# Kernel tuning notes

Hardware: AMD Instinct MI355X
Metric: run time of the kernel (lower is better)

Reference implementation:

```python
import jax, jax.numpy as jnp
import numpy as np

N_NODES = 50000
N_EDGES = 800000
NODE_DIM = 64
EDGE_DIM = 16
HIDDEN = 128
EPS = 1e-5


def _linear_init(key, fan_in, fan_out):
    k1, k2 = jax.random.split(key)
    bound = 1.0 / np.sqrt(fan_in)
    W = jax.random.uniform(k1, (fan_in, fan_out), minval=-bound, maxval=bound, dtype=jnp.float32)
    b = jax.random.uniform(k2, (fan_out,), minval=-bound, maxval=bound, dtype=jnp.float32)
    return W, b


def batchnorm(h, gamma, beta):
    # BatchNorm1d in training mode: batch mean/var (biased), eps=1e-5
    mu = jnp.mean(h, axis=0, keepdims=True)
    var = jnp.mean((h - mu) ** 2, axis=0, keepdims=True)
    return (h - mu) * jax.lax.rsqrt(var + EPS) * gamma + beta


def setup_inputs() -> dict:
    key = jax.random.key(0)
    ks = jax.random.split(key, 8)
    x = jax.random.normal(ks[0], (N_NODES, NODE_DIM), dtype=jnp.float32)
    edge_index = jax.random.randint(ks[1], (2, N_EDGES), 0, N_NODES, dtype=jnp.int64)
    edge_attr = jax.random.normal(ks[2], (N_EDGES, EDGE_DIM), dtype=jnp.float32)
    We1, be1 = _linear_init(ks[3], 2 * NODE_DIM + EDGE_DIM, HIDDEN)
    We2, be2 = _linear_init(ks[4], HIDDEN, HIDDEN)
    Wm, bm = _linear_init(ks[5], HIDDEN, HIDDEN)
    Wn1, bn1 = _linear_init(ks[6], NODE_DIM + HIDDEN, HIDDEN)
    Wn2, bn2 = _linear_init(ks[7], HIDDEN, HIDDEN)
    ones = jnp.ones((HIDDEN,), jnp.float32)
    zeros = jnp.zeros((HIDDEN,), jnp.float32)
    return dict(x=x, edge_index=edge_index, edge_attr=edge_attr,
                We1=We1, be1=be1, ge=ones, bbe=zeros, We2=We2, be2=be2,
                Wm=Wm, bm=bm,
                Wn1=Wn1, bn1=bn1, gn=ones, bbn=zeros, Wn2=Wn2, bn2=bn2)


def reference(x, edge_index, edge_attr, We1, be1, ge, bbe, We2, be2, Wm, bm, Wn1, bn1, gn, bbn, Wn2, bn2):
    row, col = edge_index[0], edge_index[1]
    # gather + concat -> edge network (Linear, BN, ReLU, Linear)
    edge_input = jnp.concatenate([x[row], x[col], edge_attr], axis=-1)  # [E, 2n+e]
    h = jax.nn.relu(batchnorm(edge_input @ We1 + be1, ge, bbe))
    edge_features = h @ We2 + be2
    # message MLP (Linear, ReLU)
    messages = jax.nn.relu(edge_features @ Wm + bm)  # [E, H]
    # scatter-add into source nodes
    agg = jax.ops.segment_sum(messages, row, num_segments=N_NODES)  # [N, H]
    # node network (Linear, BN, ReLU, Linear)
    node_input = jnp.concatenate([x, agg], axis=-1)
    hn = jax.nn.relu(batchnorm(node_input @ Wn1 + bn1, gn, bbn))
    return hn @ Wn2 + bn2
```

## Files before the change

kernel.cpp:

```cpp
#include <hip/hip_runtime.h>
#include <stdint.h>

#define NNODES 50000
#define NEDGES 800000
#define H 128
#define BN_EPS 1e-5f

typedef short short8 __attribute__((ext_vector_type(8)));
typedef short short4v __attribute__((ext_vector_type(4)));
typedef float f32x4 __attribute__((ext_vector_type(4)));

__device__ __forceinline__ float bf2f(unsigned short u) {
    unsigned int v = ((unsigned int)u) << 16;
    return __uint_as_float(v);
}
__device__ __forceinline__ unsigned short f2bf(float f) {
    unsigned int x = __float_as_uint(f);
    return (unsigned short)((x + 0x7FFFu + ((x >> 16) & 1u)) >> 16);
}
__device__ __forceinline__ short8 s8z() { short8 z = {0,0,0,0,0,0,0,0}; return z; }

template<int KB>
__device__ __forceinline__ void gemm_tile(const short* __restrict__ sA, const int SK,
                                          const unsigned short* __restrict__ WT, const int RK,
                                          const int n0, f32x4 acc[4][4], const int lane) {
    const int mr = lane & 15, quad = lane >> 4;
    const short* W = (const short*)WT;
    #pragma unroll
    for (int kb = 0; kb < KB; ++kb) {
        short8 a[4];
        #pragma unroll
        for (int mt = 0; mt < 4; ++mt)
            a[mt] = *(const short8*)&sA[(mt*16 + mr)*SK + kb*32 + quad*8];
        #pragma unroll
        for (int nt = 0; nt < 4; ++nt) {
            short8 b = *(const short8*)&W[(size_t)(n0 + nt*16 + mr)*RK + kb*32 + quad*8];
            #pragma unroll
            for (int mt = 0; mt < 4; ++mt)
                acc[mt][nt] = __builtin_amdgcn_mfma_f32_16x16x32_bf16(a[mt], b, acc[mt][nt], 0, 0, 0);
        }
    }
}

__global__ void k_fold(const float* __restrict__ We2, const float* __restrict__ be2,
                       const float* __restrict__ Wm, const float* __restrict__ bm,
                       float* __restrict__ W2m, float* __restrict__ b2m) {
    int j = threadIdx.x;
    int i = blockIdx.x;
    if (i < H) {
        float acc = 0.f;
        for (int k = 0; k < H; ++k) acc = fmaf(We2[i*H + k], Wm[k*H + j], acc);
        W2m[i*H + j] = acc;
    } else {
        float acc = bm[j];
        for (int k = 0; k < H; ++k) acc = fmaf(be2[k], Wm[k*H + j], acc);
        b2m[j] = acc;
    }
}

__global__ void k_prep2(const float* __restrict__ We1, const float* __restrict__ Wn1,
                        const float* __restrict__ Wn2,
                        unsigned short* __restrict__ WabT, unsigned short* __restrict__ Wn1T,
                        unsigned short* __restrict__ Wn2T, unsigned short* __restrict__ WcT,
                        int* __restrict__ cnt, float* __restrict__ S1f) {
    int i = blockIdx.x*256 + threadIdx.x;
    if (i < 16384) {
        int n = i >> 6, k = i & 63;
        WabT[n*64 + k] = f2bf(We1[(n < 128 ? k : 64 + k)*H + (n & 127)]);
    } else if (i < 40960) {
        int j = i - 16384; int n = j / 192, k = j - n*192;
        Wn1T[n*192 + k] = f2bf(Wn1[k*H + n]);
    } else if (i < 57344) {
        int j = i - 40960; int n = j >> 7, k = j & 127;
        Wn2T[n*H + k] = f2bf(Wn2[k*H + n]);
    } else if (i < 61440) {
        int j = i - 57344; int n = j >> 5, k = j & 31;
        WcT[n*32 + k] = (k < 16) ? f2bf(We1[(128 + k)*H + n]) : (unsigned short)0;
    } else if (i < 111440) {
        cnt[i - 61440] = 0;
    } else if (i < 112464) {
        S1f[i - 111440] = 0.f;
    }
}

__global__ void k_count(const int* __restrict__ ei, int* __restrict__ cnt) {
    int e = blockIdx.x*256 + threadIdx.x;
    if (e < NEDGES) atomicAdd(&cnt[ei[e]], 1);
}

__global__ void k_scanA(const int* __restrict__ cnt, int* __restrict__ bsum) {
    __shared__ int ws[4];
    const int tid = threadIdx.x;
    int i = blockIdx.x*256 + tid;
    int v = (i < NNODES) ? cnt[i] : 0;
    #pragma unroll
    for (int off = 32; off > 0; off >>= 1) v += __shfl_down(v, off);
    if ((tid & 63) == 0) ws[tid >> 6] = v;
    __syncthreads();
    if (tid == 0) bsum[blockIdx.x] = ws[0] + ws[1] + ws[2] + ws[3];
}

__global__ void k_scanB(const int* __restrict__ bsum, int* __restrict__ bpre,
                        int* __restrict__ offsets) {
    __shared__ int ws[4];
    const int tid = threadIdx.x;
    const int lane = tid & 63, wid = tid >> 6;
    int v = (tid < 196) ? bsum[tid] : 0;
    int xv = v;
    #pragma unroll
    for (int off = 1; off < 64; off <<= 1) {
        int y = __shfl_up(xv, off);
        if (lane >= off) xv += y;
    }
    if (lane == 63) ws[wid] = xv;
    __syncthreads();
    int base = 0;
    for (int w = 0; w < 4; ++w) if (w < wid) base += ws[w];
    int incl = base + xv;
    if (tid < 196) bpre[tid] = incl - v;
    if (tid == 255) offsets[NNODES] = incl;
}

__global__ void k_scanC(const int* __restrict__ cnt, const int* __restrict__ bpre,
                        int* __restrict__ offsets, int* __restrict__ cursor) {
    __shared__ int ws[4];
    const int tid = threadIdx.x;
    const int lane = tid & 63, wid = tid >> 6;
    int i = blockIdx.x*256 + tid;
    int v = (i < NNODES) ? cnt[i] : 0;
    int xv = v;
    #pragma unroll
    for (int off = 1; off < 64; off <<= 1) {
        int y = __shfl_up(xv, off);
        if (lane >= off) xv += y;
    }
    if (lane == 63) ws[wid] = xv;
    __syncthreads();
    int base = bpre[blockIdx.x];
    for (int w = 0; w < 4; ++w) if (w < wid) base += ws[w];
    int excl = base + xv - v;
    if (i < NNODES) { offsets[i] = excl; cursor[i] = excl; }
}

__global__ void k_scatter(const int* __restrict__ ei, int* __restrict__ cursor,
                          int* __restrict__ elist) {
    int e = blockIdx.x*256 + threadIdx.x;
    if (e < NEDGES) {
        int p = atomicAdd(&cursor[ei[e]], 1);
        elist[p] = e;
    }
}

__launch_bounds__(256)
__global__ void k_T(const float* __restrict__ x, const unsigned short* __restrict__ WabT,
                    unsigned short* __restrict__ T) {
    __shared__ short sA[128*72];
    const int tid = threadIdx.x;
    const int n0b = blockIdx.x*128;
    {
        const int rowl = tid >> 1, half = (tid & 1)*32;
        const int node = n0b + rowl;
        const bool ok = node < NNODES;
        #pragma unroll
        for (int c = 0; c < 4; ++c) {
            int k0 = half + c*8;
            short8 o = s8z();
            if (ok) {
                float4 a = *(const float4*)&x[node*64 + k0];
                float4 b = *(const float4*)&x[node*64 + k0 + 4];
                o[0]=(short)f2bf(a.x); o[1]=(short)f2bf(a.y); o[2]=(short)f2bf(a.z); o[3]=(short)f2bf(a.w);
                o[4]=(short)f2bf(b.x); o[5]=(short)f2bf(b.y); o[6]=(short)f2bf(b.z); o[7]=(short)f2bf(b.w);
            }
            *(short8*)&sA[rowl*72 + k0] = o;
        }
    }
    __syncthreads();
    const int wave = tid >> 6, lane = tid & 63;
    const int m0 = (wave & 1)*64;
    const int n0 = blockIdx.y*128 + (wave >> 1)*64;
    f32x4 acc[4][4];
    f32x4 z = {0.f, 0.f, 0.f, 0.f};
    #pragma unroll
    for (int mt = 0; mt < 4; ++mt)
        #pragma unroll
        for (int nt = 0; nt < 4; ++nt) acc[mt][nt] = z;
    gemm_tile<2>(sA + m0*72, 72, WabT, 64, n0, acc, lane);
    const int mr = lane & 15, quad = lane >> 4;
    #pragma unroll
    for (int nt = 0; nt < 4; ++nt) {
        int j = n0 + nt*16 + mr;
        #pragma unroll
        for (int mt = 0; mt < 4; ++mt) {
            int nb = n0b + m0 + mt*16 + quad*4;
            #pragma unroll
            for (int r = 0; r < 4; ++r) {
                int node = nb + r;
                if (node < NNODES) T[(size_t)node*256 + j] = f2bf(acc[mt][nt][r]);
            }
        }
    }
}

__launch_bounds__(256)
__global__ void k_gather3(const unsigned short* __restrict__ T, const int* __restrict__ ei,
                          const int* __restrict__ elist, const float* __restrict__ ea,
                          const unsigned short* __restrict__ WcT, const float* __restrict__ be1,
                          unsigned short* __restrict__ hb,
                          float* __restrict__ gS, float* __restrict__ gSS) {
    __shared__ short sT[128*136];
    __shared__ float sS[H], sSS[H];
    __shared__ int sE[128];
    const int tid = threadIdx.x;
    const int p0 = blockIdx.x*128;
    if (tid < 128) { sS[tid] = 0.f; sSS[tid] = 0.f; sE[tid] = elist[p0 + tid]; }
    __syncthreads();
    const int lp = tid >> 1, half = tid & 1;
    {
        const int e = sE[lp];
        const int row = ei[e], col = ei[NEDGES + e];
        #pragma unroll
        for (int c = 0; c < 8; ++c) {
            int jj = half*64 + c*8;
            short8 t1 = *(const short8*)&T[(size_t)row*256 + jj];
            short8 t2 = *(const short8*)&T[(size_t)col*256 + 128 + jj];
            short8 o;
            #pragma unroll
            for (int i = 0; i < 8; ++i)
                o[i] = (short)f2bf(bf2f((unsigned short)t1[i]) + bf2f((unsigned short)t2[i]));
            *(short8*)&sT[lp*136 + jj] = o;
        }
    }
    const int wave = tid >> 6, lane = tid & 63;
    const int mr = lane & 15, quad = lane >> 4;
    const int mbase = wave*32;
    short8 a0 = s8z(), a1 = s8z();
    if (quad < 2) {
        const float4* ea4 = (const float4*)ea;
        int e0i = sE[mbase + mr];
        int e1i = sE[mbase + 16 + mr];
        float4 u = ea4[(size_t)e0i*4 + quad*2];
        float4 v = ea4[(size_t)e0i*4 + quad*2 + 1];
        a0[0]=(short)f2bf(u.x); a0[1]=(short)f2bf(u.y); a0[2]=(short)f2bf(u.z); a0[3]=(short)f2bf(u.w);
        a0[4]=(short)f2bf(v.x); a0[5]=(short)f2bf(v.y); a0[6]=(short)f2bf(v.z); a0[7]=(short)f2bf(v.w);
        u = ea4[(size_t)e1i*4 + quad*2];
        v = ea4[(size_t)e1i*4 + quad*2 + 1];
        a1[0]=(short)f2bf(u.x); a1[1]=(short)f2bf(u.y); a1[2]=(short)f2bf(u.z); a1[3]=(short)f2bf(u.w);
        a1[4]=(short)f2bf(v.x); a1[5]=(short)f2bf(v.y); a1[6]=(short)f2bf(v.z); a1[7]=(short)f2bf(v.w);
    }
    f32x4 acc[2][8];
    f32x4 z = {0.f, 0.f, 0.f, 0.f};
    #pragma unroll
    for (int mt = 0; mt < 2; ++mt)
        #pragma unroll
        for (int nt = 0; nt < 8; ++nt) acc[mt][nt] = z;
    #pragma unroll
    for (int nt = 0; nt < 8; ++nt) {
        short8 b = *(const short8*)&WcT[(nt*16 + mr)*32 + quad*8];
        acc[0][nt] = __builtin_amdgcn_mfma_f32_16x16x32_bf16(a0, b, acc[0][nt], 0, 0, 0);
        acc[1][nt] = __builtin_amdgcn_mfma_f32_16x16x32_bf16(a1, b, acc[1][nt], 0, 0, 0);
    }
    __syncthreads();
    #pragma unroll
    for (int nt = 0; nt < 8; ++nt) {
        int j = nt*16 + mr;
        float bia = be1[j];
        float s = 0.f, ssum = 0.f;
        #pragma unroll
        for (int mt = 0; mt < 2; ++mt) {
            #pragma unroll
            for (int r = 0; r < 4; ++r) {
                int m = mbase + mt*16 + quad*4 + r;
                float v = acc[mt][nt][r] + bf2f((unsigned short)sT[m*136 + j]) + bia;
                sT[m*136 + j] = (short)f2bf(v);
                s += v; ssum += v*v;
            }
        }
        atomicAdd(&sS[j], s);
        atomicAdd(&sSS[j], ssum);
    }
    __syncthreads();
    #pragma unroll
    for (int c = 0; c < 8; ++c) {
        int k0 = half*64 + c*8;
        int kb = k0 >> 5, quadS = (k0 >> 3) & 3;
        *(short8*)&hb[((size_t)(blockIdx.x*16 + kb*4 + quadS)*128 + lp)*8] =
            *(const short8*)&sT[lp*136 + k0];
    }
    if (tid < 128) { atomicAdd(&gS[tid], sS[tid]); atomicAdd(&gSS[tid], sSS[tid]); }
}

__global__ void k_stats(const float* __restrict__ S, const float* __restrict__ SS,
                        const float* __restrict__ g, const float* __restrict__ b,
                        float invCount, float* __restrict__ scale, float* __restrict__ shift) {
    int j = threadIdx.x;
    float mu = S[j]*invCount;
    float var = SS[j]*invCount - mu*mu;
    float sc = rsqrtf(var + BN_EPS)*g[j];
    scale[j] = sc;
    shift[j] = b[j] - mu*sc;
}

__global__ void k_prep3(const float* __restrict__ W2m, const float* __restrict__ scale,
                        const float* __restrict__ shift, unsigned short* __restrict__ W2mST,
                        float* __restrict__ tvec, float* __restrict__ agg) {
    int i = blockIdx.x*256 + threadIdx.x;
    if (i < 16384) {
        int n = i >> 7, k = i & 127;
        W2mST[n*H + k] = f2bf(scale[k] * W2m[k*H + n]);
    } else if (i < 16512) {
        int k = i - 16384;
        tvec[k] = shift[k] / scale[k];
    } else if (i < 16512 + NNODES*H) {
        agg[i - 16512] = 0.f;
    }
}

__launch_bounds__(256)
__global__ void k_msgagg(const unsigned short* __restrict__ hb, const float* __restrict__ tvec,
                         const unsigned short* __restrict__ W2mST, const float* __restrict__ b2m,
                         const int* __restrict__ ei, const int* __restrict__ elist,
                         const int* __restrict__ offsets, float* __restrict__ agg) {
    __shared__ short sA[128*136];
    __shared__ int rows[128];
    __shared__ int segStart[130];
    __shared__ int wcnt[2];
    __shared__ int nsegS;
    const int tid = threadIdx.x;
    const int p0 = blockIdx.x*128;
    const int wave = tid >> 6, lane = tid & 63;
    const int mr = lane & 15, quad = lane >> 4;
    const int mbase = wave*32;
    short8 raw[4][2];
    #pragma unroll
    for (int kb = 0; kb < 4; ++kb)
        #pragma unroll
        for (int mt = 0; mt < 2; ++mt)
            raw[kb][mt] = *(const short8*)&hb[((size_t)(blockIdx.x*16 + kb*4 + quad)*128
                                              + mbase + mt*16 + mr)*8];
    int pre = 0, st = 0;
    if (tid < 128) rows[tid] = ei[elist[p0 + tid]];
    __syncthreads();
    if (tid < 128) {
        int r0 = rows[tid];
        st = (tid == 0) || (rows[tid - 1] != r0);
        unsigned long long m = __ballot(st);
        int lane2 = tid & 63;
        pre = __popcll(m & ((1ull << lane2) - 1ull));
        if (lane2 == 63) wcnt[tid >> 6] = pre + st;
    }
    __syncthreads();
    if (tid < 128) {
        int base = (tid >= 64) ? wcnt[0] : 0;
        int sid = base + pre + st - 1;
        if (st) segStart[sid] = tid;
        if (tid == 127) {
            int ns = wcnt[0] + wcnt[1];
            nsegS = ns;
            segStart[ns] = 128;
        }
    }
    f32x4 acc[2][8];
    f32x4 z = {0.f, 0.f, 0.f, 0.f};
    #pragma unroll
    for (int mt = 0; mt < 2; ++mt)
        #pragma unroll
        for (int nt = 0; nt < 8; ++nt) acc[mt][nt] = z;
    #pragma unroll
    for (int kb = 0; kb < 4; ++kb) {
        float4 tq0 = *(const float4*)&tvec[kb*32 + quad*8];
        float4 tq1 = *(const float4*)&tvec[kb*32 + quad*8 + 4];
        short8 a[2];
        #pragma unroll
        for (int mt = 0; mt < 2; ++mt) {
            short8 rw = raw[kb][mt];
            short8 av;
            av[0] = (short)f2bf(fmaxf(bf2f((unsigned short)rw[0]) + tq0.x, 0.f));
            av[1] = (short)f2bf(fmaxf(bf2f((unsigned short)rw[1]) + tq0.y, 0.f));
            av[2] = (short)f2bf(fmaxf(bf2f((unsigned short)rw[2]) + tq0.z, 0.f));
            av[3] = (short)f2bf(fmaxf(bf2f((unsigned short)rw[3]) + tq0.w, 0.f));
            av[4] = (short)f2bf(fmaxf(bf2f((unsigned short)rw[4]) + tq1.x, 0.f));
            av[5] = (short)f2bf(fmaxf(bf2f((unsigned short)rw[5]) + tq1.y, 0.f));
            av[6] = (short)f2bf(fmaxf(bf2f((unsigned short)rw[6]) + tq1.z, 0.f));
            av[7] = (short)f2bf(fmaxf(bf2f((unsigned short)rw[7]) + tq1.w, 0.f));
            a[mt] = av;
        }
        #pragma unroll
        for (int nt = 0; nt < 8; ++nt) {
            short8 b = *(const short8*)&W2mST[(nt*16 + mr)*H + kb*32 + quad*8];
            acc[0][nt] = __builtin_amdgcn_mfma_f32_16x16x32_bf16(a[0], b, acc[0][nt], 0, 0, 0);
            acc[1][nt] = __builtin_amdgcn_mfma_f32_16x16x32_bf16(a[1], b, acc[1][nt], 0, 0, 0);
        }
    }
    #pragma unroll
    for (int nt = 0; nt < 8; ++nt) {
        int j = nt*16 + mr;
        float bias = b2m[j];
        #pragma unroll
        for (int mt = 0; mt < 2; ++mt) {
            #pragma unroll
            for (int r = 0; r < 4; ++r) {
                int m = mbase + mt*16 + quad*4 + r;
                sA[m*136 + j] = (short)f2bf(fmaxf(acc[mt][nt][r] + bias, 0.f));
            }
        }
    }
    __syncthreads();
    const int nseg = nsegS;
    for (int idx = tid; idx < (nseg << 5); idx += 256) {
        int s = idx >> 5, g = idx & 31;
        int j0 = g*4;
        int a0 = segStart[s], b0 = segStart[s + 1];
        float s0 = 0.f, s1 = 0.f, s2 = 0.f, s3 = 0.f;
        for (int i = a0; i < b0; ++i) {
            short4v v = *(const short4v*)&sA[i*136 + j0];
            s0 += bf2f((unsigned short)v[0]);
            s1 += bf2f((unsigned short)v[1]);
            s2 += bf2f((unsigned short)v[2]);
            s3 += bf2f((unsigned short)v[3]);
        }
        int r = rows[a0];
        bool interior = (a0 > 0) && (b0 < 128);
        bool full = interior || ((p0 + a0 == offsets[r]) && (p0 + b0 == offsets[r + 1]));
        float* dst = &agg[(size_t)r*H + j0];
        if (full) {
            f32x4 o = {s0, s1, s2, s3};
            *(f32x4*)dst = o;
        } else {
            atomicAdd(dst + 0, s0);
            atomicAdd(dst + 1, s1);
            atomicAdd(dst + 2, s2);
            atomicAdd(dst + 3, s3);
        }
    }
}

__launch_bounds__(256)
__global__ void k_node1(const float* __restrict__ x, const float* __restrict__ agg,
                        const unsigned short* __restrict__ Wn1T, const float* __restrict__ bn1,
                        float* __restrict__ h2, float* __restrict__ gS, float* __restrict__ gSS) {
    __shared__ short sA[128*200];
    __shared__ float sS[H], sSS[H];
    const int tid = threadIdx.x;
    if (tid < H) { sS[tid] = 0.f; sSS[tid] = 0.f; }
    const int n0b = blockIdx.x*128;
    {
        const int rowl = tid >> 1, half = (tid & 1)*96;
        const int node = n0b + rowl;
        const bool ok = node < NNODES;
        #pragma unroll
        for (int c = 0; c < 12; ++c) {
            int k0 = half + c*8;
            short8 o = s8z();
            if (ok) {
                float4 a, b;
                if (k0 < 64) {
                    a = *(const float4*)&x[node*64 + k0];
                    b = *(const float4*)&x[node*64 + k0 + 4];
                } else {
                    a = *(const float4*)&agg[(size_t)node*H + (k0 - 64)];
                    b = *(const float4*)&agg[(size_t)node*H + (k0 - 64) + 4];
                }
                o[0]=(short)f2bf(a.x); o[1]=(short)f2bf(a.y); o[2]=(short)f2bf(a.z); o[3]=(short)f2bf(a.w);
                o[4]=(short)f2bf(b.x); o[5]=(short)f2bf(b.y); o[6]=(short)f2bf(b.z); o[7]=(short)f2bf(b.w);
            }
            *(short8*)&sA[rowl*200 + k0] = o;
        }
    }
    __syncthreads();
    const int wave = tid >> 6, lane = tid & 63;
    const int m0 = (wave & 1)*64, n0 = (wave >> 1)*64;
    f32x4 acc[4][4];
    f32x4 z = {0.f, 0.f, 0.f, 0.f};
    #pragma unroll
    for (int mt = 0; mt < 4; ++mt)
        #pragma unroll
        for (int nt = 0; nt < 4; ++nt) acc[mt][nt] = z;
    gemm_tile<6>(sA + m0*200, 200, Wn1T, 192, n0, acc, lane);
    const int mr = lane & 15, quad = lane >> 4;
    #pragma unroll
    for (int nt = 0; nt < 4; ++nt) {
        int j = n0 + nt*16 + mr;
        float bias = bn1[j];
        float s = 0.f, ssum = 0.f;
        #pragma unroll
        for (int mt = 0; mt < 4; ++mt) {
            int nb = n0b + m0 + mt*16 + quad*4;
            #pragma unroll
            for (int r = 0; r < 4; ++r) {
                int node = nb + r;
                if (node < NNODES) {
                    float v = acc[mt][nt][r] + bias;
                    h2[(size_t)node*H + j] = v;
                    s += v; ssum += v*v;
                }
            }
        }
        atomicAdd(&sS[j], s);
        atomicAdd(&sSS[j], ssum);
    }
    __syncthreads();
    if (tid < H) { atomicAdd(&gS[tid], sS[tid]); atomicAdd(&gSS[tid], sSS[tid]); }
}

__launch_bounds__(256)
__global__ void k_node2(const float* __restrict__ h2, const float* __restrict__ scale,
                        const float* __restrict__ shift, const unsigned short* __restrict__ Wn2T,
                        const float* __restrict__ bn2, float* __restrict__ out) {
    __shared__ short sA[128*136];
    const int tid = threadIdx.x;
    const int n0b = blockIdx.x*128;
    {
        const int rowl = tid >> 1, half = (tid & 1)*64;
        const int node = n0b + rowl;
        const bool ok = node < NNODES;
        #pragma unroll
        for (int c = 0; c < 8; ++c) {
            int k0 = half + c*8;
            short8 o = s8z();
            if (ok) {
                float4 a = *(const float4*)&h2[(size_t)node*H + k0];
                float4 b = *(const float4*)&h2[(size_t)node*H + k0 + 4];
                float4 sc0 = *(const float4*)&scale[k0], sc1 = *(const float4*)&scale[k0 + 4];
                float4 sh0 = *(const float4*)&shift[k0], sh1 = *(const float4*)&shift[k0 + 4];
                o[0] = (short)f2bf(fmaxf(fmaf(a.x, sc0.x, sh0.x), 0.f));
                o[1] = (short)f2bf(fmaxf(fmaf(a.y, sc0.y, sh0.y), 0.f));
                o[2] = (short)f2bf(fmaxf(fmaf(a.z, sc0.z, sh0.z), 0.f));
                o[3] = (short)f2bf(fmaxf(fmaf(a.w, sc0.w, sh0.w), 0.f));
                o[4] = (short)f2bf(fmaxf(fmaf(b.x, sc1.x, sh1.x), 0.f));
                o[5] = (short)f2bf(fmaxf(fmaf(b.y, sc1.y, sh1.y), 0.f));
                o[6] = (short)f2bf(fmaxf(fmaf(b.z, sc1.z, sh1.z), 0.f));
                o[7] = (short)f2bf(fmaxf(fmaf(b.w, sc1.w, sh1.w), 0.f));
            }
            *(short8*)&sA[rowl*136 + k0] = o;
        }
    }
    __syncthreads();
    const int wave = tid >> 6, lane = tid & 63;
    const int m0 = (wave & 1)*64, n0 = (wave >> 1)*64;
    f32x4 acc[4][4];
    f32x4 z = {0.f, 0.f, 0.f, 0.f};
    #pragma unroll
    for (int mt = 0; mt < 4; ++mt)
        #pragma unroll
        for (int nt = 0; nt < 4; ++nt) acc[mt][nt] = z;
    gemm_tile<4>(sA + m0*136, 136, Wn2T, 128, n0, acc, lane);
    const int mr = lane & 15, quad = lane >> 4;
    #pragma unroll
    for (int nt = 0; nt < 4; ++nt) {
        int j = n0 + nt*16 + mr;
        float bias = bn2[j];
        #pragma unroll
        for (int mt = 0; mt < 4; ++mt) {
            int nb = n0b + m0 + mt*16 + quad*4;
            #pragma unroll
            for (int r = 0; r < 4; ++r) {
                int node = nb + r;
                if (node < NNODES) out[(size_t)node*H + j] = acc[mt][nt][r] + bias;
            }
        }
    }
}

extern "C" void kernel_launch(void* const* d_in, const int* in_sizes, int n_in,
                              void* d_out, int out_size, void* d_ws, size_t ws_size,
                              hipStream_t stream) {
    (void)in_sizes; (void)n_in; (void)out_size; (void)ws_size;
    const float* x   = (const float*)d_in[0];
    const int*   ei  = (const int*)d_in[1];
    const float* ea  = (const float*)d_in[2];
    const float* We1 = (const float*)d_in[3];
    const float* be1 = (const float*)d_in[4];
    const float* ge  = (const float*)d_in[5];
    const float* bbe = (const float*)d_in[6];
    const float* We2 = (const float*)d_in[7];
    const float* be2 = (const float*)d_in[8];
    const float* Wm  = (const float*)d_in[9];
    const float* bm  = (const float*)d_in[10];
    const float* Wn1 = (const float*)d_in[11];
    const float* bn1 = (const float*)d_in[12];
    const float* gn  = (const float*)d_in[13];
    const float* bbn = (const float*)d_in[14];
    const float* Wn2 = (const float*)d_in[15];
    const float* bn2 = (const float*)d_in[16];
    float* out = (float*)d_out;

    char* ws = (char*)d_ws;
    unsigned short* hb   = (unsigned short*)(ws);
    float*          h2   = (float*)(ws);
    float*          agg  = (float*)(ws + 204800000);
    unsigned short* Tbuf = (unsigned short*)(ws + 230400000);
    int* cnt     = (int*)(ws + 256000000);
    int* offsets = (int*)(ws + 256200192);
    int* cursor  = (int*)(ws + 256400448);
    int* bsum    = (int*)(ws + 256600448);
    int* bpre    = (int*)(ws + 256601472);
    int* elist   = (int*)(ws + 256602496);
    float* S1     = (float*)(ws + 259802496);
    float* SS1    = S1 + 128;
    float* S2     = S1 + 256;
    float* SS2    = S1 + 384;
    float* scale1 = S1 + 512;
    float* shift1 = S1 + 640;
    float* scale2 = S1 + 768;
    float* shift2 = S1 + 896;
    float* W2m  = (float*)(ws + 259806592);
    float* b2m  = (float*)(ws + 259872128);
    float* tvec = (float*)(ws + 259872640);
    unsigned short* WabT  = (unsigned short*)(ws + 259873152);
    unsigned short* Wn1T  = (unsigned short*)(ws + 259905920);
    unsigned short* Wn2T  = (unsigned short*)(ws + 259955072);
    unsigned short* W2mST = (unsigned short*)(ws + 259987840);
    unsigned short* WcT   = (unsigned short*)(ws + 260020608);

    k_fold<<<H + 1, H, 0, stream>>>(We2, be2, Wm, bm, W2m, b2m);
    k_prep2<<<440, 256, 0, stream>>>(We1, Wn1, Wn2, WabT, Wn1T, Wn2T, WcT, cnt, S1);
    k_count<<<NEDGES/256, 256, 0, stream>>>(ei, cnt);
    k_scanA<<<196, 256, 0, stream>>>(cnt, bsum);
    k_scanB<<<1, 256, 0, stream>>>(bsum, bpre, offsets);
    k_scanC<<<196, 256, 0, stream>>>(cnt, bpre, offsets, cursor);
    k_scatter<<<NEDGES/256, 256, 0, stream>>>(ei, cursor, elist);
    k_T<<<dim3(391, 2), 256, 0, stream>>>(x, WabT, Tbuf);
    k_gather3<<<NEDGES/128, 256, 0, stream>>>(Tbuf, ei, elist, ea, WcT, be1, hb, S1, SS1);
    k_stats<<<1, H, 0, stream>>>(S1, SS1, ge, bbe, 1.0f/NEDGES, scale1, shift1);
    k_prep3<<<12565, 256, 0, stream>>>(W2m, scale1, shift1, W2mST, tvec, agg);
    k_msgagg<<<NEDGES/128, 256, 0, stream>>>(hb, tvec, W2mST, b2m, ei, elist, offsets, agg);
    k_node1<<<391, 256, 0, stream>>>(x, agg, Wn1T, bn1, h2, S2, SS2);
    k_stats<<<1, H, 0, stream>>>(S2, SS2, gn, bbn, 1.0f/NNODES, scale2, shift2);
    k_node2<<<391, 256, 0, stream>>>(h2, scale2, shift2, Wn2T, bn2, out);
}
```

Measured before the change: 665.0 us.

## Batch gather loads, drop LDS edge list, shuffle-reduce BN stats, nontemporal hb traffic

The gather kernel no longer stages the edge list in shared memory behind a barrier. It reads elist directly, issues the edge-attr loads first, and hoists all sixteen T row loads ahead of the adds so more memory requests are in flight. The per-column BN partial sums are now reduced across quads with shuffles before the shared atomics, which cuts LDS atomic contention by four. The hb intermediate is written and read with nontemporal hints, and launch bounds request 4 blocks per CU, which may raise register pressure or cause spills.

```diff
diff --git a/kernel.cpp b/kernel.cpp
--- a/kernel.cpp
+++ b/kernel.cpp
@@ -201,7 +201,7 @@
     }
 }
 
-__launch_bounds__(256)
+__launch_bounds__(256, 4)
 __global__ void k_gather3(const unsigned short* __restrict__ T, const int* __restrict__ ei,
                           const int* __restrict__ elist, const float* __restrict__ ea,
                           const unsigned short* __restrict__ WcT, const float* __restrict__ be1,
@@ -209,43 +209,43 @@
                           float* __restrict__ gS, float* __restrict__ gSS) {
     __shared__ short sT[128*136];
     __shared__ float sS[H], sSS[H];
-    __shared__ int sE[128];
     const int tid = threadIdx.x;
     const int p0 = blockIdx.x*128;
-    if (tid < 128) { sS[tid] = 0.f; sSS[tid] = 0.f; sE[tid] = elist[p0 + tid]; }
-    __syncthreads();
-    const int lp = tid >> 1, half = tid & 1;
-    {
-        const int e = sE[lp];
-        const int row = ei[e], col = ei[NEDGES + e];
-        #pragma unroll
-        for (int c = 0; c < 8; ++c) {
-            int jj = half*64 + c*8;
-            short8 t1 = *(const short8*)&T[(size_t)row*256 + jj];
-            short8 t2 = *(const short8*)&T[(size_t)col*256 + 128 + jj];
-            short8 o;
-            #pragma unroll
-            for (int i = 0; i < 8; ++i)
-                o[i] = (short)f2bf(bf2f((unsigned short)t1[i]) + bf2f((unsigned short)t2[i]));
-            *(short8*)&sT[lp*136 + jj] = o;
-        }
-    }
     const int wave = tid >> 6, lane = tid & 63;
     const int mr = lane & 15, quad = lane >> 4;
     const int mbase = wave*32;
+    if (tid < 128) { sS[tid] = 0.f; sSS[tid] = 0.f; }
     short8 a0 = s8z(), a1 = s8z();
     if (quad < 2) {
-        const float4* ea4 = (const float4*)ea;
-        int e0i = sE[mbase + mr];
-        int e1i = sE[mbase + 16 + mr];
-        float4 u = ea4[(size_t)e0i*4 + quad*2];
-        float4 v = ea4[(size_t)e0i*4 + quad*2 + 1];
-        a0[0]=(short)f2bf(u.x); a0[1]=(short)f2bf(u.y); a0[2]=(short)f2bf(u.z); a0[3]=(short)f2bf(u.w);
-        a0[4]=(short)f2bf(v.x); a0[5]=(short)f2bf(v.y); a0[6]=(short)f2bf(v.z); a0[7]=(short)f2bf(v.w);
-        u = ea4[(size_t)e1i*4 + quad*2];
-        v = ea4[(size_t)e1i*4 + quad*2 + 1];
-        a1[0]=(short)f2bf(u.x); a1[1]=(short)f2bf(u.y); a1[2]=(short)f2bf(u.z); a1[3]=(short)f2bf(u.w);
-        a1[4]=(short)f2bf(v.x); a1[5]=(short)f2bf(v.y); a1[6]=(short)f2bf(v.z); a1[7]=(short)f2bf(v.w);
+        int e0i = elist[p0 + mbase + mr];
+        int e1i = elist[p0 + mbase + 16 + mr];
+        f32x4 u0 = __builtin_nontemporal_load((const f32x4*)&ea[(size_t)e0i*16 + quad*8]);
+        f32x4 u1 = __builtin_nontemporal_load((const f32x4*)&ea[(size_t)e0i*16 + quad*8 + 4]);
+        f32x4 v0 = __builtin_nontemporal_load((const f32x4*)&ea[(size_t)e1i*16 + quad*8]);
+        f32x4 v1 = __builtin_nontemporal_load((const f32x4*)&ea[(size_t)e1i*16 + quad*8 + 4]);
+        a0[0]=(short)f2bf(u0[0]); a0[1]=(short)f2bf(u0[1]); a0[2]=(short)f2bf(u0[2]); a0[3]=(short)f2bf(u0[3]);
+        a0[4]=(short)f2bf(u1[0]); a0[5]=(short)f2bf(u1[1]); a0[6]=(short)f2bf(u1[2]); a0[7]=(short)f2bf(u1[3]);
+        a1[0]=(short)f2bf(v0[0]); a1[1]=(short)f2bf(v0[1]); a1[2]=(short)f2bf(v0[2]); a1[3]=(short)f2bf(v0[3]);
+        a1[4]=(short)f2bf(v1[0]); a1[5]=(short)f2bf(v1[1]); a1[6]=(short)f2bf(v1[2]); a1[7]=(short)f2bf(v1[3]);
+    }
+    const int lp = tid >> 1, half = tid & 1;
+    const int e = elist[p0 + lp];
+    const int row = ei[e], col = ei[NEDGES + e];
+    const unsigned short* Tr = &T[(size_t)row*256 + half*64];
+    const unsigned short* Tc = &T[(size_t)col*256 + 128 + half*64];
+    short8 t1[8], t2[8];
+    #pragma unroll
+    for (int c = 0; c < 8; ++c) {
+        t1[c] = *(const short8*)&Tr[c*8];
+        t2[c] = *(const short8*)&Tc[c*8];
+    }
+    #pragma unroll
+    for (int c = 0; c < 8; ++c) {
+        short8 o;
+        #pragma unroll
+        for (int i = 0; i < 8; ++i)
+            o[i] = (short)f2bf(bf2f((unsigned short)t1[c][i]) + bf2f((unsigned short)t2[c][i]));
+        *(short8*)&sT[lp*136 + half*64 + c*8] = o;
     }
     f32x4 acc[2][8];
     f32x4 z = {0.f, 0.f, 0.f, 0.f};
@@ -275,16 +275,23 @@
                 s += v; ssum += v*v;
             }
         }
-        atomicAdd(&sS[j], s);
-        atomicAdd(&sSS[j], ssum);
+        s += __shfl_xor(s, 16);
+        ssum += __shfl_xor(ssum, 16);
+        s += __shfl_xor(s, 32);
+        ssum += __shfl_xor(ssum, 32);
+        if (quad == 0) {
+            atomicAdd(&sS[j], s);
+            atomicAdd(&sSS[j], ssum);
+        }
     }
     __syncthreads();
     #pragma unroll
     for (int c = 0; c < 8; ++c) {
         int k0 = half*64 + c*8;
         int kb = k0 >> 5, quadS = (k0 >> 3) & 3;
-        *(short8*)&hb[((size_t)(blockIdx.x*16 + kb*4 + quadS)*128 + lp)*8] =
-            *(const short8*)&sT[lp*136 + k0];
+        short8 v = *(const short8*)&sT[lp*136 + k0];
+        __builtin_nontemporal_store(v,
+            (short8*)&hb[((size_t)(blockIdx.x*16 + kb*4 + quadS)*128 + lp)*8]);
     }
     if (tid < 128) { atomicAdd(&gS[tid], sS[tid]); atomicAdd(&gSS[tid], sSS[tid]); }
 }
@@ -335,8 +342,9 @@
     for (int kb = 0; kb < 4; ++kb)
         #pragma unroll
         for (int mt = 0; mt < 2; ++mt)
-            raw[kb][mt] = *(const short8*)&hb[((size_t)(blockIdx.x*16 + kb*4 + quad)*128
-                                              + mbase + mt*16 + mr)*8];
+            raw[kb][mt] = __builtin_nontemporal_load(
+                (const short8*)&hb[((size_t)(blockIdx.x*16 + kb*4 + quad)*128
+                                    + mbase + mt*16 + mr)*8]);
     int pre = 0, st = 0;
     if (tid < 128) rows[tid] = ei[elist[p0 + tid]];
     __syncthreads();
```

New measurement: 654.8 us. Within noise of the previous version (-1.5%).
